# Kernel optimization log

Measured on AMD Instinct MI355X. Metric: run time of the kernel, lower is better.

## Reference

```python
import jax, jax.numpy as jnp
import numpy as np

H = 16
D_MODEL = 1024
D_K = D_MODEL // H
SEQ = 2048
BATCH = 2


def setup_inputs() -> dict:
    key = jax.random.key(0)
    ks = jax.random.split(key, 11)
    s = 1.0 / np.sqrt(D_MODEL)
    inp = {
        "query": jax.random.normal(ks[0], (SEQ, BATCH, D_MODEL), jnp.float32),
        "key_": jax.random.normal(ks[1], (SEQ, BATCH, D_MODEL), jnp.float32),
        "value": jax.random.normal(ks[2], (SEQ, BATCH, D_MODEL), jnp.float32),
        "Wq": jax.random.uniform(ks[3], (D_MODEL, D_MODEL), jnp.float32, -s, s),
        "bq": jax.random.uniform(ks[4], (D_MODEL,), jnp.float32, -s, s),
        "Wk": jax.random.uniform(ks[5], (D_MODEL, D_MODEL), jnp.float32, -s, s),
        "bk": jax.random.uniform(ks[6], (D_MODEL,), jnp.float32, -s, s),
        "Wv": jax.random.uniform(ks[7], (D_MODEL, D_MODEL), jnp.float32, -s, s),
        "bv": jax.random.uniform(ks[8], (D_MODEL,), jnp.float32, -s, s),
        "Wo": jax.random.uniform(ks[9], (D_MODEL, D_MODEL), jnp.float32, -s, s),
        "bo": jax.random.uniform(ks[10], (D_MODEL,), jnp.float32, -s, s),
    }
    return inp


def _mha(query, key_, value, Wq, bq, Wk, bk, Wv, bv, Wo, bo):
    S, B, D = query.shape
    # torch Linear: x @ W.T + b; then view(S,B,h,dk).transpose(0,2) -> [h,B,S,dk]
    def proj(x, W, b):
        return jnp.transpose((x @ W.T + b).reshape(S, B, H, D_K), (2, 1, 0, 3))

    q = proj(query, Wq, bq)   # [h, b, S, dk]
    k = proj(key_, Wk, bk)
    v = proj(value, Wv, bv)

    scores = jnp.einsum("hbqd,hbkd->hbqk", q, k) / jnp.sqrt(
        jnp.asarray(D_K, q.dtype)
    )  # [h, b, S, S]
    p_attn = jax.nn.softmax(scores, axis=-1)  # dropout p=0.0 -> identity
    x = jnp.einsum("hbqk,hbkd->hbqd", p_attn, v)  # [h, b, S, dk]
    x = jnp.transpose(x, (2, 1, 0, 3)).reshape(S, B, D)  # back to [S, B, D]
    return x @ Wo.T + bo


def reference(query, key_, value, Wq, bq, Wk, bk, Wv, bv, Wo, bo):
    return _mha(query, key_, value, Wq, bq, Wk, bk, Wv, bv, Wo, bo)
```

## Files before the change

### kernel.cpp

```cpp
#include <hip/hip_runtime.h>

#define SEQ   2048
#define BATCH 2
#define DM    1024
#define NH    16
#define DKD   64
#define MROWS (SEQ*BATCH)

using bf16x8 = __attribute__((ext_vector_type(8))) __bf16;
using bf16x4 = __attribute__((ext_vector_type(4))) __bf16;
using bf16x2 = __attribute__((ext_vector_type(2))) __bf16;
using f32x4  = __attribute__((ext_vector_type(4))) float;

__device__ __forceinline__ void gld_lds16(const __bf16* g, __bf16* l) {
  __builtin_amdgcn_global_load_lds(
      (__attribute__((address_space(1))) void*)(g),
      (__attribute__((address_space(3))) void*)(l), 16, 0, 0);
}

__global__ __launch_bounds__(256) void cvt_all(
    const float* __restrict__ s0, const float* __restrict__ s1,
    const float* __restrict__ s2, const float* __restrict__ s3,
    const float* __restrict__ s4, const float* __restrict__ s5,
    const float* __restrict__ s6,
    __bf16* __restrict__ d0, __bf16* __restrict__ d1, __bf16* __restrict__ d2,
    __bf16* __restrict__ d3, __bf16* __restrict__ d4, __bf16* __restrict__ d5,
    __bf16* __restrict__ d6, int n_big, int n_small) {
  int y = blockIdx.y;
  const float* s; __bf16* d;
  switch (y) {
    case 0: s = s0; d = d0; break;
    case 1: s = s1; d = d1; break;
    case 2: s = s2; d = d2; break;
    case 3: s = s3; d = d3; break;
    case 4: s = s4; d = d4; break;
    case 5: s = s5; d = d5; break;
    default: s = s6; d = d6; break;
  }
  int n = (y < 3) ? n_big : n_small;
  int i = (blockIdx.x * 256 + threadIdx.x) * 8;
  if (i >= n) return;
  const float4* sp = (const float4*)(s + i);
  float4 a = sp[0], b = sp[1];
  bf16x8 v;
  v[0]=(__bf16)a.x; v[1]=(__bf16)a.y; v[2]=(__bf16)a.z; v[3]=(__bf16)a.w;
  v[4]=(__bf16)b.x; v[5]=(__bf16)b.y; v[6]=(__bf16)b.z; v[7]=(__bf16)b.w;
  *(bf16x8*)(d + i) = v;
}

__device__ __forceinline__ void gemm_core(const __bf16* __restrict__ A,
                                          const __bf16* __restrict__ Bt,
                                          __bf16* Ash, __bf16* Bsh,
                                          f32x4 acc[4][4], int m0, int n0) {
  const int K = DM;
  int tid = threadIdx.x;
  int lane = tid & 63, quad = lane >> 4, l16 = lane & 15;
  int w = tid >> 6;
  int wm = (w & 1) * 64, wn = (w >> 1) * 64;
  for (int k0 = 0; k0 < K; k0 += 32) {
    __syncthreads();
#pragma unroll
    for (int it = 0; it < 2; ++it) {
      int c   = tid + it * 256;
      int row = c >> 2, ko = (c & 3) * 8;
      int base = (tid - lane + it * 256) * 8;
      gld_lds16(A  + (size_t)(m0 + row) * K + k0 + ko, Ash + base);
      gld_lds16(Bt + (size_t)(n0 + row) * K + k0 + ko, Bsh + base);
    }
    __syncthreads();
    bf16x8 af[4], bfr[4];
#pragma unroll
    for (int mi = 0; mi < 4; mi++)
      af[mi] = *(const bf16x8*)&Ash[(wm + mi * 16 + l16) * 32 + quad * 8];
#pragma unroll
    for (int ni = 0; ni < 4; ni++)
      bfr[ni] = *(const bf16x8*)&Bsh[(wn + ni * 16 + l16) * 32 + quad * 8];
#pragma unroll
    for (int mi = 0; mi < 4; mi++)
#pragma unroll
      for (int ni = 0; ni < 4; ni++)
        acc[mi][ni] = __builtin_amdgcn_mfma_f32_16x16x32_bf16(
            af[mi], bfr[ni], acc[mi][ni], 0, 0, 0);
  }
}

__global__ __launch_bounds__(256, 2) void gemm_qkv(
    const __bf16* __restrict__ Xq, const __bf16* __restrict__ Xk,
    const __bf16* __restrict__ Xv, const __bf16* __restrict__ Wqkv,
    const float* __restrict__ bqp, const float* __restrict__ bkp,
    const float* __restrict__ bvp,
    __bf16* __restrict__ Qb, __bf16* __restrict__ Kb, __bf16* __restrict__ Vt) {
  __shared__ __bf16 Ash[128 * 32], Bsh[128 * 32];
  __shared__ __bf16 Esh[4][16 * 72];
  int z = blockIdx.z;
  const __bf16* A   = (z == 0) ? Xq : (z == 1) ? Xk : Xv;
  const __bf16* Bt  = Wqkv + (size_t)z * (DM * DM);
  const float* bias = (z == 0) ? bqp : (z == 1) ? bkp : bvp;
  int m0 = blockIdx.y * 128, n0 = blockIdx.x * 128;
  f32x4 acc[4][4] = {};
  gemm_core(A, Bt, Ash, Bsh, acc, m0, n0);

  int tid = threadIdx.x, lane = tid & 63, quad = lane >> 4, l16 = lane & 15;
  int w = tid >> 6, wm = (w & 1) * 64, wn = (w >> 1) * 64;
  __bf16* E = Esh[w];
  int n_base = n0 + wn;
  int hh = n_base >> 6;
  float bb[4];
#pragma unroll
  for (int ni = 0; ni < 4; ni++) bb[ni] = bias[n_base + ni * 16 + l16];

  if (z == 2) {
#pragma unroll
    for (int ni = 0; ni < 4; ni++) {
#pragma unroll
      for (int mi = 0; mi < 4; mi++) {
        int s0 = mi * 8 + quad * 2;
        bf16x2 p0, p1;
        p0[0] = (__bf16)(acc[mi][ni][0] + bb[ni]);
        p0[1] = (__bf16)(acc[mi][ni][2] + bb[ni]);
        p1[0] = (__bf16)(acc[mi][ni][1] + bb[ni]);
        p1[1] = (__bf16)(acc[mi][ni][3] + bb[ni]);
        *(bf16x2*)&E[l16 * 72 + s0]      = p0;
        *(bf16x2*)&E[l16 * 72 + 32 + s0] = p1;
      }
      asm volatile("s_waitcnt lgkmcnt(0)" ::: "memory");
#pragma unroll
      for (int pass = 0; pass < 2; pass++) {
        int ddl = pass * 8 + (lane >> 3);
        int col = (lane & 7) * 8;
        bf16x8 v = *(const bf16x8*)&E[ddl * 72 + col];
        int b2 = col >> 5, sl = col & 31;
        int dd = ni * 16 + ddl;
        int sg = ((m0 + wm) >> 1) + sl;
        *(bf16x8*)&Vt[(((size_t)hh * BATCH + b2) * DKD + dd) * SEQ + sg] = v;
      }
      asm volatile("s_waitcnt lgkmcnt(0)" ::: "memory");
    }
  } else {
    __bf16* Out = (z == 0) ? Qb : Kb;
#pragma unroll
    for (int mi = 0; mi < 4; mi++) {
#pragma unroll
      for (int ni = 0; ni < 4; ni++)
#pragma unroll
        for (int r = 0; r < 4; r++)
          E[(quad * 4 + r) * 72 + ni * 16 + l16] =
              (__bf16)(acc[mi][ni][r] + bb[ni]);
      asm volatile("s_waitcnt lgkmcnt(0)" ::: "memory");
#pragma unroll
      for (int pass = 0; pass < 2; pass++) {
        int row16 = pass * 8 + (lane >> 3);
        int coll  = (lane & 7) * 8;
        bf16x8 v = *(const bf16x8*)&E[row16 * 72 + coll];
        int m = m0 + wm + mi * 16 + row16;
        int s = m >> 1, b2 = m & 1;
        *(bf16x8*)&Out[(((size_t)hh * BATCH + b2) * SEQ + s) * DKD + coll] = v;
      }
      asm volatile("s_waitcnt lgkmcnt(0)" ::: "memory");
    }
  }
}

__global__ __launch_bounds__(256, 2) void gemm_out(
    const __bf16* __restrict__ A, const __bf16* __restrict__ Bt,
    const float* __restrict__ bias, float* __restrict__ out) {
  __shared__ __bf16 Ash[128 * 32], Bsh[128 * 32];
  int m0 = blockIdx.y * 128, n0 = blockIdx.x * 128;
  f32x4 acc[4][4] = {};
  gemm_core(A, Bt, Ash, Bsh, acc, m0, n0);

  int tid = threadIdx.x, lane = tid & 63, quad = lane >> 4, l16 = lane & 15;
  int w = tid >> 6, wm = (w & 1) * 64, wn = (w >> 1) * 64;
#pragma unroll
  for (int ni = 0; ni < 4; ni++) {
    int n = n0 + wn + ni * 16 + l16;
    float bb = bias[n];
#pragma unroll
    for (int mi = 0; mi < 4; mi++) {
#pragma unroll
      for (int r = 0; r < 4; r++) {
        int m = m0 + wm + mi * 16 + quad * 4 + r;
        out[(size_t)m * DM + n] = acc[mi][ni][r] + bb;
      }
    }
  }
}

__global__ __launch_bounds__(128, 2) void flash_attn(
    const __bf16* __restrict__ Qg, const __bf16* __restrict__ Kg,
    const __bf16* __restrict__ Vtg, __bf16* __restrict__ Xa) {
  __shared__ __bf16 Ksh[2][64 * 64];
  __shared__ __bf16 Vsh[2][64 * 64];
  __shared__ __bf16 Psh[2][32 * 64];
  int tid = threadIdx.x, w = tid >> 6, lane = tid & 63;
  int quad = lane >> 4, l16 = lane & 15, sw = l16 & 7;
  int h = blockIdx.z, b = blockIdx.y, q0 = blockIdx.x * 64;
  size_t hb = ((size_t)h * BATCH + b) * SEQ * DKD;
  const __bf16* Qp = Qg + hb;
  const __bf16* Kp = Kg + hb;
  const __bf16* Vp = Vtg + hb;
  __bf16* Pw = Psh[w];

  bf16x8 qf[2][2];
#pragma unroll
  for (int qb = 0; qb < 2; qb++)
#pragma unroll
    for (int kk = 0; kk < 2; kk++)
      qf[qb][kk] = *(const bf16x8*)(
          Qp + (size_t)(q0 + w * 32 + qb * 16 + l16) * DKD + kk * 32 + quad * 8);

  f32x4 o[2][4] = {};
  float l_[2] = {0.f, 0.f};
  const float c1 = 0.18033688011112042f;
  const float SHIFT = 4.0f;

#pragma unroll
  for (int it = 0; it < 4; ++it) {
    int c = tid + it * 128;
    int r = c >> 3, pp = c & 7;
    int off = (pp ^ (r & 7)) << 3;
    gld_lds16(Kp + (size_t)r * DKD + off, Ksh[0] + c * 8);
    gld_lds16(Vp + (size_t)r * SEQ + off, Vsh[0] + c * 8);
  }

  for (int t = 0; t < SEQ / 64; ++t) {
    __syncthreads();
    if (t + 1 < SEQ / 64) {
      int k0n = (t + 1) * 64, bn = (t + 1) & 1;
#pragma unroll
      for (int it = 0; it < 4; ++it) {
        int c = tid + it * 128;
        int r = c >> 3, pp = c & 7;
        int off = (pp ^ (r & 7)) << 3;
        gld_lds16(Kp + (size_t)(k0n + r) * DKD + off, Ksh[bn] + c * 8);
        gld_lds16(Vp + (size_t)r * SEQ + k0n + off, Vsh[bn] + c * 8);
      }
    }
    const __bf16* Kb_ = Ksh[t & 1];
    const __bf16* Vb_ = Vsh[t & 1];

    f32x4 sc[2][4];
#pragma unroll
    for (int ji = 0; ji < 4; ji++) {
      int rr = ji * 16 + l16;
      bf16x8 kf0 = *(const bf16x8*)&Kb_[rr * 64 + ((quad ^ sw) << 3)];
      bf16x8 kf1 = *(const bf16x8*)&Kb_[rr * 64 + (((4 + quad) ^ sw) << 3)];
#pragma unroll
      for (int qb = 0; qb < 2; qb++) {
        f32x4 t2 = {0.f, 0.f, 0.f, 0.f};
        t2 = __builtin_amdgcn_mfma_f32_16x16x32_bf16(kf0, qf[qb][0], t2, 0, 0, 0);
        t2 = __builtin_amdgcn_mfma_f32_16x16x32_bf16(kf1, qf[qb][1], t2, 0, 0, 0);
        sc[qb][ji] = t2;
      }
    }

#pragma unroll
    for (int qb = 0; qb < 2; qb++) {
      float rs = 0.f;
#pragma unroll
      for (int ji = 0; ji < 4; ji++) {
        bf16x4 pk;
#pragma unroll
        for (int r = 0; r < 4; r++) {
          float pv = exp2f(sc[qb][ji][r] * c1 - SHIFT);
          rs += pv;
          pk[r] = (__bf16)pv;
        }
        *(bf16x4*)&Pw[(qb * 16 + l16) * 64 +
                      (((ji * 2 + (quad >> 1)) ^ sw) << 3) + ((quad & 1) << 2)] = pk;
      }
      rs += __shfl_xor(rs, 16, 64);
      rs += __shfl_xor(rs, 32, 64);
      l_[qb] += rs;
    }

#pragma unroll
    for (int kk = 0; kk < 2; kk++) {
      bf16x8 pa[2];
#pragma unroll
      for (int qb = 0; qb < 2; qb++)
        pa[qb] = *(const bf16x8*)&Pw[(qb * 16 + l16) * 64 +
                                     (((kk * 4 + quad) ^ sw) << 3)];
#pragma unroll
      for (int ni = 0; ni < 4; ni++) {
        int rr = ni * 16 + l16;
        bf16x8 vb = *(const bf16x8*)&Vb_[rr * 64 + (((kk * 4 + quad) ^ sw) << 3)];
#pragma unroll
        for (int qb = 0; qb < 2; qb++)
          o[qb][ni] = __builtin_amdgcn_mfma_f32_16x16x32_bf16(pa[qb], vb,
                                                              o[qb][ni], 0, 0, 0);
      }
    }
  }

#pragma unroll
  for (int qb = 0; qb < 2; qb++)
#pragma unroll
    for (int r = 0; r < 4; r++) {
      float li = 1.0f / __shfl(l_[qb], quad * 4 + r, 64);
      int q = q0 + w * 32 + qb * 16 + quad * 4 + r;
#pragma unroll
      for (int ni = 0; ni < 4; ni++) {
        int d = ni * 16 + l16;
        Xa[((size_t)q * BATCH + b) * DM + h * DKD + d] =
            (__bf16)(o[qb][ni][r] * li);
      }
    }
}

extern "C" void kernel_launch(void* const* d_in, const int* in_sizes, int n_in,
                              void* d_out, int out_size, void* d_ws,
                              size_t ws_size, hipStream_t stream) {
  (void)in_sizes; (void)n_in; (void)out_size; (void)ws_size;
  const float* query = (const float*)d_in[0];
  const float* key_  = (const float*)d_in[1];
  const float* value = (const float*)d_in[2];
  const float* Wq = (const float*)d_in[3];
  const float* bq = (const float*)d_in[4];
  const float* Wk = (const float*)d_in[5];
  const float* bk = (const float*)d_in[6];
  const float* Wv = (const float*)d_in[7];
  const float* bv = (const float*)d_in[8];
  const float* Wo = (const float*)d_in[9];
  const float* bo = (const float*)d_in[10];

  const size_t NX = (size_t)MROWS * DM;
  const size_t NW = (size_t)DM * DM;
  __bf16* p    = (__bf16*)d_ws;
  __bf16* Xq   = p; p += NX;
  __bf16* Xk   = p; p += NX;
  __bf16* Xv   = p; p += NX;
  __bf16* Wqkv = p; p += 3 * NW;
  __bf16* Wob  = p; p += NW;
  __bf16* Qb   = p; p += NX;
  __bf16* Kb   = p; p += NX;
  __bf16* Vt   = p; p += NX;
  __bf16* Xa   = p; p += NX;

  cvt_all<<<dim3((unsigned)(NX / 2048), 7), 256, 0, stream>>>(
      query, key_, value, Wq, Wk, Wv, Wo,
      Xq, Xk, Xv, Wqkv, Wqkv + NW, Wqkv + 2 * NW, Wob, (int)NX, (int)NW);

  gemm_qkv<<<dim3(DM / 128, MROWS / 128, 3), 256, 0, stream>>>(
      Xq, Xk, Xv, Wqkv, bq, bk, bv, Qb, Kb, Vt);
  flash_attn<<<dim3(SEQ / 64, BATCH, NH), 128, 0, stream>>>(Qb, Kb, Vt, Xa);
  gemm_out<<<dim3(DM / 128, MROWS / 128), 256, 0, stream>>>(
      Xa, Wob, bo, (float*)d_out);
}
```

Baseline: 250.4 us.

## Use four waves per attention block and smaller M tiles in output GEMM

Flash attention now runs 256 threads per block, each wave owning 16 query rows instead of 32. That doubles the waves sharing each K/V tile and lowers per-wave register pressure. The output GEMM switches to 64x128 tiles with an inlined loop, doubling its grid to fill more CUs, and occupancy hints for the GEMMs go up from 2 to 3. The cost is less per-wave reuse of the K/V fragments loaded from LDS and more block-level synchronisation per unit of work.

```diff
diff --git a/kernel.cpp b/kernel.cpp
--- a/kernel.cpp
+++ b/kernel.cpp
@@ -84,7 +84,7 @@
   }
 }
 
-__global__ __launch_bounds__(256, 2) void gemm_qkv(
+__global__ __launch_bounds__(256, 3) void gemm_qkv(
     const __bf16* __restrict__ Xq, const __bf16* __restrict__ Xk,
     const __bf16* __restrict__ Xv, const __bf16* __restrict__ Wqkv,
     const float* __restrict__ bqp, const float* __restrict__ bkp,
@@ -161,22 +161,53 @@
   }
 }
 
-__global__ __launch_bounds__(256, 2) void gemm_out(
+__global__ __launch_bounds__(256, 3) void gemm_out(
     const __bf16* __restrict__ A, const __bf16* __restrict__ Bt,
     const float* __restrict__ bias, float* __restrict__ out) {
-  __shared__ __bf16 Ash[128 * 32], Bsh[128 * 32];
-  int m0 = blockIdx.y * 128, n0 = blockIdx.x * 128;
-  f32x4 acc[4][4] = {};
-  gemm_core(A, Bt, Ash, Bsh, acc, m0, n0);
-
-  int tid = threadIdx.x, lane = tid & 63, quad = lane >> 4, l16 = lane & 15;
-  int w = tid >> 6, wm = (w & 1) * 64, wn = (w >> 1) * 64;
+  __shared__ __bf16 Ash[64 * 32], Bsh[128 * 32];
+  const int K = DM;
+  int m0 = blockIdx.y * 64, n0 = blockIdx.x * 128;
+  int tid = threadIdx.x;
+  int lane = tid & 63, quad = lane >> 4, l16 = lane & 15;
+  int w = tid >> 6;
+  int wm = (w & 1) * 32, wn = (w >> 1) * 64;
+  f32x4 acc[2][4] = {};
+  for (int k0 = 0; k0 < K; k0 += 32) {
+    __syncthreads();
+    {
+      int c = tid;
+      int row = c >> 2, ko = (c & 3) * 8;
+      gld_lds16(A + (size_t)(m0 + row) * K + k0 + ko,
+                Ash + (tid - lane) * 8);
+    }
+#pragma unroll
+    for (int it = 0; it < 2; ++it) {
+      int c = tid + it * 256;
+      int row = c >> 2, ko = (c & 3) * 8;
+      gld_lds16(Bt + (size_t)(n0 + row) * K + k0 + ko,
+                Bsh + (tid - lane + it * 256) * 8);
+    }
+    __syncthreads();
+    bf16x8 af[2], bfr[4];
+#pragma unroll
+    for (int mi = 0; mi < 2; mi++)
+      af[mi] = *(const bf16x8*)&Ash[(wm + mi * 16 + l16) * 32 + quad * 8];
+#pragma unroll
+    for (int ni = 0; ni < 4; ni++)
+      bfr[ni] = *(const bf16x8*)&Bsh[(wn + ni * 16 + l16) * 32 + quad * 8];
+#pragma unroll
+    for (int mi = 0; mi < 2; mi++)
+#pragma unroll
+      for (int ni = 0; ni < 4; ni++)
+        acc[mi][ni] = __builtin_amdgcn_mfma_f32_16x16x32_bf16(
+            af[mi], bfr[ni], acc[mi][ni], 0, 0, 0);
+  }
 #pragma unroll
   for (int ni = 0; ni < 4; ni++) {
     int n = n0 + wn + ni * 16 + l16;
     float bb = bias[n];
 #pragma unroll
-    for (int mi = 0; mi < 4; mi++) {
+    for (int mi = 0; mi < 2; mi++) {
 #pragma unroll
       for (int r = 0; r < 4; r++) {
         int m = m0 + wm + mi * 16 + quad * 4 + r;
@@ -186,12 +217,12 @@
   }
 }
 
-__global__ __launch_bounds__(128, 2) void flash_attn(
+__global__ __launch_bounds__(256, 4) void flash_attn(
     const __bf16* __restrict__ Qg, const __bf16* __restrict__ Kg,
     const __bf16* __restrict__ Vtg, __bf16* __restrict__ Xa) {
   __shared__ __bf16 Ksh[2][64 * 64];
   __shared__ __bf16 Vsh[2][64 * 64];
-  __shared__ __bf16 Psh[2][32 * 64];
+  __shared__ __bf16 Psh[4][16 * 64];
   int tid = threadIdx.x, w = tid >> 6, lane = tid & 63;
   int quad = lane >> 4, l16 = lane & 15, sw = l16 & 7;
   int h = blockIdx.z, b = blockIdx.y, q0 = blockIdx.x * 64;
@@ -201,22 +232,20 @@
   const __bf16* Vp = Vtg + hb;
   __bf16* Pw = Psh[w];
 
-  bf16x8 qf[2][2];
-#pragma unroll
-  for (int qb = 0; qb < 2; qb++)
-#pragma unroll
-    for (int kk = 0; kk < 2; kk++)
-      qf[qb][kk] = *(const bf16x8*)(
-          Qp + (size_t)(q0 + w * 32 + qb * 16 + l16) * DKD + kk * 32 + quad * 8);
-
-  f32x4 o[2][4] = {};
-  float l_[2] = {0.f, 0.f};
+  bf16x8 qf[2];
+#pragma unroll
+  for (int kk = 0; kk < 2; kk++)
+    qf[kk] = *(const bf16x8*)(
+        Qp + (size_t)(q0 + w * 16 + l16) * DKD + kk * 32 + quad * 8);
+
+  f32x4 o[4] = {};
+  float l_ = 0.f;
   const float c1 = 0.18033688011112042f;
   const float SHIFT = 4.0f;
 
 #pragma unroll
-  for (int it = 0; it < 4; ++it) {
-    int c = tid + it * 128;
+  for (int it = 0; it < 2; ++it) {
+    int c = tid + it * 256;
     int r = c >> 3, pp = c & 7;
     int off = (pp ^ (r & 7)) << 3;
     gld_lds16(Kp + (size_t)r * DKD + off, Ksh[0] + c * 8);
@@ -228,8 +257,8 @@
     if (t + 1 < SEQ / 64) {
       int k0n = (t + 1) * 64, bn = (t + 1) & 1;
 #pragma unroll
-      for (int it = 0; it < 4; ++it) {
-        int c = tid + it * 128;
+      for (int it = 0; it < 2; ++it) {
+        int c = tid + it * 256;
         int r = c >> 3, pp = c & 7;
         int off = (pp ^ (r & 7)) << 3;
         gld_lds16(Kp + (size_t)(k0n + r) * DKD + off, Ksh[bn] + c * 8);
@@ -239,73 +268,60 @@
     const __bf16* Kb_ = Ksh[t & 1];
     const __bf16* Vb_ = Vsh[t & 1];
 
-    f32x4 sc[2][4];
+    f32x4 sc[4];
 #pragma unroll
     for (int ji = 0; ji < 4; ji++) {
       int rr = ji * 16 + l16;
       bf16x8 kf0 = *(const bf16x8*)&Kb_[rr * 64 + ((quad ^ sw) << 3)];
       bf16x8 kf1 = *(const bf16x8*)&Kb_[rr * 64 + (((4 + quad) ^ sw) << 3)];
-#pragma unroll
-      for (int qb = 0; qb < 2; qb++) {
-        f32x4 t2 = {0.f, 0.f, 0.f, 0.f};
-        t2 = __builtin_amdgcn_mfma_f32_16x16x32_bf16(kf0, qf[qb][0], t2, 0, 0, 0);
-        t2 = __builtin_amdgcn_mfma_f32_16x16x32_bf16(kf1, qf[qb][1], t2, 0, 0, 0);
-        sc[qb][ji] = t2;
-      }
-    }
-
-#pragma unroll
-    for (int qb = 0; qb < 2; qb++) {
+      f32x4 t2 = {0.f, 0.f, 0.f, 0.f};
+      t2 = __builtin_amdgcn_mfma_f32_16x16x32_bf16(kf0, qf[0], t2, 0, 0, 0);
+      t2 = __builtin_amdgcn_mfma_f32_16x16x32_bf16(kf1, qf[1], t2, 0, 0, 0);
+      sc[ji] = t2;
+    }
+
+    {
       float rs = 0.f;
 #pragma unroll
       for (int ji = 0; ji < 4; ji++) {
         bf16x4 pk;
 #pragma unroll
         for (int r = 0; r < 4; r++) {
-          float pv = exp2f(sc[qb][ji][r] * c1 - SHIFT);
+          float pv = exp2f(sc[ji][r] * c1 - SHIFT);
           rs += pv;
           pk[r] = (__bf16)pv;
         }
-        *(bf16x4*)&Pw[(qb * 16 + l16) * 64 +
+        *(bf16x4*)&Pw[l16 * 64 +
                       (((ji * 2 + (quad >> 1)) ^ sw) << 3) + ((quad & 1) << 2)] = pk;
       }
       rs += __shfl_xor(rs, 16, 64);
       rs += __shfl_xor(rs, 32, 64);
-      l_[qb] += rs;
+      l_ += rs;
     }
 
 #pragma unroll
     for (int kk = 0; kk < 2; kk++) {
-      bf16x8 pa[2];
-#pragma unroll
-      for (int qb = 0; qb < 2; qb++)
-        pa[qb] = *(const bf16x8*)&Pw[(qb * 16 + l16) * 64 +
-                                     (((kk * 4 + quad) ^ sw) << 3)];
+      bf16x8 pa = *(const bf16x8*)&Pw[l16 * 64 + (((kk * 4 + quad) ^ sw) << 3)];
 #pragma unroll
       for (int ni = 0; ni < 4; ni++) {
         int rr = ni * 16 + l16;
         bf16x8 vb = *(const bf16x8*)&Vb_[rr * 64 + (((kk * 4 + quad) ^ sw) << 3)];
-#pragma unroll
-        for (int qb = 0; qb < 2; qb++)
-          o[qb][ni] = __builtin_amdgcn_mfma_f32_16x16x32_bf16(pa[qb], vb,
-                                                              o[qb][ni], 0, 0, 0);
-      }
-    }
-  }
-
-#pragma unroll
-  for (int qb = 0; qb < 2; qb++)
-#pragma unroll
-    for (int r = 0; r < 4; r++) {
-      float li = 1.0f / __shfl(l_[qb], quad * 4 + r, 64);
-      int q = q0 + w * 32 + qb * 16 + quad * 4 + r;
-#pragma unroll
-      for (int ni = 0; ni < 4; ni++) {
-        int d = ni * 16 + l16;
-        Xa[((size_t)q * BATCH + b) * DM + h * DKD + d] =
-            (__bf16)(o[qb][ni][r] * li);
-      }
-    }
+        o[ni] = __builtin_amdgcn_mfma_f32_16x16x32_bf16(pa, vb, o[ni], 0, 0, 0);
+      }
+    }
+  }
+
+#pragma unroll
+  for (int r = 0; r < 4; r++) {
+    float li = 1.0f / __shfl(l_, quad * 4 + r, 64);
+    int q = q0 + w * 16 + quad * 4 + r;
+#pragma unroll
+    for (int ni = 0; ni < 4; ni++) {
+      int d = ni * 16 + l16;
+      Xa[((size_t)q * BATCH + b) * DM + h * DKD + d] =
+          (__bf16)(o[ni][r] * li);
+    }
+  }
 }
 
 extern "C" void kernel_launch(void* const* d_in, const int* in_sizes, int n_in,
@@ -343,7 +359,7 @@
 
   gemm_qkv<<<dim3(DM / 128, MROWS / 128, 3), 256, 0, stream>>>(
       Xq, Xk, Xv, Wqkv, bq, bk, bv, Qb, Kb, Vt);
-  flash_attn<<<dim3(SEQ / 64, BATCH, NH), 128, 0, stream>>>(Qb, Kb, Vt, Xa);
-  gemm_out<<<dim3(DM / 128, MROWS / 128), 256, 0, stream>>>(
+  flash_attn<<<dim3(SEQ / 64, BATCH, NH), 256, 0, stream>>>(Qb, Kb, Vt, Xa);
+  gemm_out<<<dim3(DM / 128, MROWS / 64), 256, 0, stream>>>(
       Xa, Wob, bo, (float*)d_out);
 }
```

Result: faster. 240.6 us (-3.9%).
